# Performance work log

Measured on AMD Instinct MI355X. Metric: run time of the kernel, lower is better.

Reference implementation:

```python
import jax, jax.numpy as jnp
import numpy as np

K = 20          # knn neighbors (args.k)
BN_EPS = 1e-5   # torch BatchNorm default
LN_EPS = 1e-6


def _bn(x, g, b, axes):
    # training-mode batchnorm over `axes`, channel dim = 1
    m = x.mean(axes, keepdims=True)
    v = x.var(axes, keepdims=True)
    shp = [1] * x.ndim
    shp[1] = x.shape[1]
    return g.reshape(shp) * (x - m) * jax.lax.rsqrt(v + BN_EPS) + b.reshape(shp)


def _lrelu(x):
    return jnp.where(x >= 0, x, 0.2 * x)


def _graph_feature(x, k):
    # x: [B,C,N] -> [B,2C,N,k]  (knn gather + (neighbor-center, center) concat)
    B, C, N = x.shape
    inner = -2.0 * jnp.einsum('bcn,bcm->bnm', x, x)
    xx = jnp.sum(x * x, axis=1)                       # [B,N]
    pd = -xx[:, :, None] - inner - xx[:, None, :]     # negative sq. distance
    idx = jax.lax.top_k(pd, k)[1]                     # [B,N,k]
    xt = jnp.transpose(x, (0, 2, 1))                  # [B,N,C]
    feat = xt[jnp.arange(B)[:, None, None], idx]      # [B,N,k,C] gather
    ctr = xt[:, :, None, :]
    out = jnp.concatenate([feat - ctr, jnp.broadcast_to(ctr, feat.shape)], axis=-1)
    return jnp.transpose(out, (0, 3, 1, 2))


def _conv2d_block(x, w, g, b):
    # 1x1 conv2d (no bias) + BN2d + LeakyReLU(0.2)
    y = jnp.einsum('bcnk,oc->bonk', x, w)
    return _lrelu(_bn(y, g, b, (0, 2, 3)))


def _conv1d_block(x, w, g, b):
    y = jnp.einsum('bcl,oc->bol', x, w)
    return _lrelu(_bn(y, g, b, (0, 2)))


def _squash(t):
    sn = jnp.sum(t * t, axis=-1, keepdims=True)
    return sn * t / ((1.0 + sn) * jnp.sqrt(sn))


def _forward(data, l, dw1, dg1, db1, dw2, dg2, db2, dw3, dg3, db3,
             lin_w, ln_w, ln_b, caps_W,
             cw1, cg1, cb1, cw2, cg2, cb2, cw3, cw4, cg4, cb4, cw5, cg5, cb5):
    B, _, N = data.shape
    # ---- DGCNN encoder ----
    x = _conv2d_block(_graph_feature(data, K), dw1, dg1, db1)
    x1 = x.max(axis=-1)                               # [B,64,N]
    x = _conv2d_block(_graph_feature(x1, K), dw2, dg2, db2)
    x2 = x.max(axis=-1)                               # [B,64,N]
    x = _conv2d_block(_graph_feature(x2, K), dw3, dg3, db3)
    x3 = x.max(axis=-1)                               # [B,128,N]
    feat = jnp.transpose(jnp.concatenate([x1, x2, x3], axis=1), (0, 2, 1))  # [B,N,256]
    h = jnp.einsum('bnc,oc->bno', feat, lin_w)        # [B,N,40]
    mu = h.mean(axis=(1, 2), keepdims=True)
    var = h.var(axis=(1, 2), keepdims=True)
    encoder = jax.nn.relu(ln_w * (h - mu) * jax.lax.rsqrt(var + LN_EPS) + ln_b)  # [B,1024,40]
    # ---- Latent capsule layer (3-iter dynamic routing) ----
    u_hat = jnp.einsum('lpvd,bpd->blpv', caps_W, encoder)  # [B,40,1024,64]
    u_det = jax.lax.stop_gradient(u_hat)
    b_ij = jnp.zeros((B, caps_W.shape[0], caps_W.shape[1]), encoder.dtype)
    v = None
    for it in range(3):
        c = jax.nn.softmax(b_ij, axis=1)
        if it == 2:
            v = _squash(jnp.einsum('blp,blpv->blv', c, u_hat))
        else:
            v = _squash(jnp.einsum('blp,blpv->blv', c, u_det))
            b_ij = b_ij + jnp.einsum('blv,blpv->blp', v, u_det)
    latent = v                                        # [B,40,64]
    # ---- segmentation head ----
    emb = jnp.einsum('bpd,bdv->bpv', encoder, latent) # [B,1024,64]
    emb = emb.max(axis=-1, keepdims=True)             # [B,1024,1]
    lab = _conv1d_block(l.reshape(B, -1, 1), cw1, cg1, cb1)  # [B,64,1]
    emb = jnp.concatenate([emb, lab], axis=1)         # [B,1088,1]
    emb = jnp.tile(emb, (1, 1, N))                    # [B,1088,N]
    emb = jnp.concatenate([emb, jnp.transpose(encoder, (0, 2, 1))], axis=1)  # [B,1128,N]
    r = _conv1d_block(emb, cw2, cg2, cb2)
    r = _conv1d_block(r, cw3, cg2, cb2)               # conv3 shares bn2 params
    r = _conv1d_block(r, cw4, cg4, cb4)
    r = _conv1d_block(r, cw5, cg5, cb5)
    return r                                          # [B,50,N]


def setup_inputs() -> dict:
    key = jax.random.key(0)
    ks = jax.random.split(key, 16)
    B, N = 32, 1024
    f = jnp.float32
    rn = lambda k, s: 0.05 * jax.random.normal(k, s, dtype=f)
    return dict(
        data=jax.random.normal(ks[0], (B, 3, N), dtype=f),
        l=jax.random.uniform(ks[1], (B, 16), dtype=f),
        dw1=rn(ks[2], (64, 6)), dg1=jnp.ones(64, f), db1=jnp.zeros(64, f),
        dw2=rn(ks[3], (64, 128)), dg2=jnp.ones(64, f), db2=jnp.zeros(64, f),
        dw3=rn(ks[4], (128, 128)), dg3=jnp.ones(128, f), db3=jnp.zeros(128, f),
        lin_w=rn(ks[5], (40, 256)),
        ln_w=jnp.ones((N, 40), f), ln_b=jnp.zeros((N, 40), f),
        caps_W=0.01 * jax.random.normal(ks[6], (40, 1024, 64, 40), dtype=f),
        cw1=rn(ks[7], (64, 16)), cg1=jnp.ones(64, f), cb1=jnp.zeros(64, f),
        cw2=rn(ks[8], (256, 1128)), cg2=jnp.ones(256, f), cb2=jnp.zeros(256, f),
        cw3=rn(ks[9], (256, 256)),
        cw4=rn(ks[10], (128, 256)), cg4=jnp.ones(128, f), cb4=jnp.zeros(128, f),
        cw5=rn(ks[11], (50, 128)), cg5=jnp.ones(50, f), cb5=jnp.zeros(50, f),
    )


def reference(data, l, dw1, dg1, db1, dw2, dg2, db2, dw3, dg3, db3,
              lin_w, ln_w, ln_b, caps_W,
              cw1, cg1, cb1, cw2, cg2, cb2, cw3, cw4, cg4, cb4, cw5, cg5, cb5):
    return _forward(data, l, dw1, dg1, db1, dw2, dg2, db2, dw3, dg3, db3,
                    lin_w, ln_w, ln_b, caps_W,
                    cw1, cg1, cb1, cw2, cg2, cb2, cw3, cw4, cg4, cb4, cw5, cg5, cb5)
```

## Files before the change

kernel.cpp:

```cpp
#include <hip/hip_runtime.h>
#include <math.h>

constexpr int NB = 32, NN = 1024, KNN = 20;
constexpr int RTOT = NB * NN;

constexpr size_t SZ_BIG = (size_t)NB * NN * 40 * 64;
constexpr size_t O_BIG  = 0;
constexpr size_t O_XT0  = O_BIG + SZ_BIG;
constexpr size_t O_XT1  = O_XT0 + (size_t)RTOT * 4;
constexpr size_t O_XT2  = O_XT1 + (size_t)RTOT * 64;
constexpr size_t O_XT3  = O_XT2 + (size_t)RTOT * 64;
constexpr size_t O_XX   = O_XT3 + (size_t)RTOT * 128;
constexpr size_t O_IDX  = O_XX + RTOT;
constexpr size_t O_WC1  = O_IDX + (size_t)RTOT * KNN;
constexpr size_t O_WC2  = O_WC1 + 512;
constexpr size_t O_WC3  = O_WC2 + 8192;
constexpr size_t O_LWT  = O_WC3 + 16384;
constexpr size_t O_C2T  = O_LWT + 16384;
constexpr size_t O_C3T  = O_C2T + 10240;
constexpr size_t O_C4T  = O_C3T + 65536;
constexpr size_t O_C5T  = O_C4T + 32768;
constexpr size_t O_H    = O_C5T + 8192;
constexpr size_t O_LNST = O_H + (size_t)RTOT * 64;
constexpr size_t O_BSUM = O_LNST + 64;
constexpr size_t O_BSQ  = O_BSUM + 256;
constexpr size_t O_SCL  = O_BSQ + 256;
constexpr size_t O_SHF  = O_SCL + 256;
constexpr size_t O_SACC = O_SHF + 256;
constexpr size_t O_VB   = O_SACC + 81920;
constexpr size_t O_BIJ  = O_VB + 81920;
constexpr size_t O_EMB  = O_BIJ + (size_t)NB * 40 * NN;
constexpr size_t O_LAB  = O_EMB + RTOT;
constexpr size_t O_BASE = O_LAB + 2048;
constexpr size_t O_PS   = O_BIJ;
constexpr size_t O_PQ   = O_BIJ + 262144;
constexpr size_t O_PB   = O_XT1;

__device__ __forceinline__ float lrelu(float z) { return fmaxf(z, 0.2f * z); }

__device__ __forceinline__ float key2f(unsigned u)
{
    unsigned b = (u & 0x80000000u) ? (u ^ 0x80000000u) : ~u;
    return __uint_as_float(b);
}

__global__ void k_wt(const float* __restrict__ src, float* __restrict__ dst,
                     int K, int On, int SS, int coff, int DS, int ooff, int Oreal)
{
    int i = blockIdx.x * 256 + threadIdx.x;
    if (i >= K * On) return;
    int c = i / On, o = i - c * On;
    dst[(size_t)c * DS + ooff + o] = (o < Oreal) ? src[(size_t)o * SS + coff + c] : 0.f;
}

__global__ void k_data_t(const float* __restrict__ d, float* __restrict__ xt)
{
    int i = blockIdx.x * 256 + threadIdx.x;
    if (i >= RTOT) return;
    int b = i >> 10, n = i & 1023;
#pragma unroll
    for (int c = 0; c < 3; ++c) xt[(size_t)i * 4 + c] = d[((size_t)b * 3 + c) * NN + n];
    xt[(size_t)i * 4 + 3] = 0.f;
}

template<int C, int CS>
__global__ void k_rownorm(const float* __restrict__ X, float* __restrict__ xx)
{
    int i = blockIdx.x * 256 + threadIdx.x;
    if (i >= RTOT) return;
    const float* p = X + (size_t)i * CS;
    float s = 0.f;
#pragma unroll
    for (int c = 0; c < C; ++c) s = fmaf(p[c], p[c], s);
    xx[i] = s;
}

template<int CS>
__global__ __launch_bounds__(256) void k_dist(const float* __restrict__ X,
    const float* __restrict__ xx, float* __restrict__ D)
{
    __shared__ float As[16][68];
    __shared__ float Bs[16][68];
    int b = blockIdx.z;
    int r0 = blockIdx.x * 64, m0 = blockIdx.y * 64;
    const float* Xb = X + (size_t)b * NN * CS;
    int t = threadIdx.x;
    int tx = t & 15, ty = t >> 4;
    float acc[4][4] = {};
    for (int k0 = 0; k0 < CS; k0 += 16) {
        __syncthreads();
        {
            int row = t >> 2, kb = (t & 3) * 4;
#pragma unroll
            for (int u = 0; u < 4; ++u) {
                int k = k0 + kb + u;
                As[kb + u][row] = (k < CS) ? Xb[(size_t)(r0 + row) * CS + k] : 0.f;
                Bs[kb + u][row] = (k < CS) ? Xb[(size_t)(m0 + row) * CS + k] : 0.f;
            }
        }
        __syncthreads();
#pragma unroll
        for (int k = 0; k < 16; ++k) {
            float4 a = *(const float4*)&As[k][ty * 4];
            float4 bb = *(const float4*)&Bs[k][tx * 4];
            float av[4] = {a.x, a.y, a.z, a.w};
            float bv[4] = {bb.x, bb.y, bb.z, bb.w};
#pragma unroll
            for (int i = 0; i < 4; ++i)
#pragma unroll
                for (int j = 0; j < 4; ++j)
                    acc[i][j] = fmaf(av[i], bv[j], acc[i][j]);
        }
    }
    const float* xxb = xx + b * NN + m0 + tx * 4;
    float x0 = xxb[0], x1 = xxb[1], x2 = xxb[2], x3 = xxb[3];
#pragma unroll
    for (int i = 0; i < 4; ++i) {
        float4 o4 = make_float4(2.f * acc[i][0] - x0, 2.f * acc[i][1] - x1,
                                2.f * acc[i][2] - x2, 2.f * acc[i][3] - x3);
        *(float4*)&D[((size_t)b * NN + r0 + ty * 4 + i) * NN + m0 + tx * 4] = o4;
    }
}

__global__ __launch_bounds__(256) void k_sel(const float* __restrict__ D,
                                             int* __restrict__ idxb)
{
    int gw = blockIdx.x * 4 + (threadIdx.x >> 6);
    int lane = threadIdx.x & 63;
    const float* drow = D + (size_t)gw * NN;
    float vr[16];
#pragma unroll
    for (int j = 0; j < 16; ++j) vr[j] = drow[j * 64 + lane];

    unsigned lo = 0x007FFFFFu;
    unsigned hi = 0xFF800000u;
#pragma unroll 1
    while (hi - lo > 1u) {
        unsigned mid = lo + ((hi - lo) >> 1);
        float tm = key2f(mid);
        int c = 0;
#pragma unroll
        for (int j = 0; j < 16; ++j) c += __popcll(__ballot(vr[j] > tm));
        if (c < KNN) hi = mid; else lo = mid;
    }
    float t = key2f(hi);

    int* outp = idxb + (size_t)gw * KNN;
    unsigned long long mylow = (1ull << lane) - 1ull;
    int base = 0;
#pragma unroll
    for (int j = 0; j < 16; ++j) {
        unsigned long long bmask = __ballot(vr[j] > t);
        if (vr[j] > t) outp[base + __popcll(bmask & mylow)] = j * 64 + lane;
        base += __popcll(bmask);
    }
#pragma unroll 1
    for (int j = 0; j < 16 && base < KNN; ++j) {
        unsigned long long bmask = __ballot(vr[j] == t);
        int pre = __popcll(bmask & mylow);
        if (vr[j] == t && base + pre < KNN) outp[base + pre] = j * 64 + lane;
        base += __popcll(bmask);
    }
}

template<bool ACT, bool BIAS>
__global__ __launch_bounds__(256) void k_gemm(const float* __restrict__ X,
    const float* __restrict__ W, float* __restrict__ Y, int K, int OC, int XS,
    const float* __restrict__ scale, const float* __restrict__ shift,
    const float* __restrict__ bias)
{
    __shared__ float Xs[16][68];
    __shared__ float Ws[16][64];
    int r0 = blockIdx.x * 64, o0 = blockIdx.y * 64;
    int t = threadIdx.x;
    int tx = t & 15, ty = t >> 4;
    float acc[4][4] = {};
    for (int k0 = 0; k0 < K; k0 += 16) {
        __syncthreads();
        {
            int row = t >> 2, kb = (t & 3) * 4;
#pragma unroll
            for (int u = 0; u < 4; ++u) {
                int k = k0 + kb + u;
                float v = 0.f;
                if (k < K) {
                    v = X[(size_t)(r0 + row) * XS + k];
                    if (ACT) { float z = fmaf(v, scale[k], shift[k]); v = fmaxf(z, 0.2f * z); }
                }
                Xs[kb + u][row] = v;
// ... 31 lines not shown
        *(float4*)&Y[(size_t)r * OC + o0 + tx * 4] = o4;
    }
}

template<int O>
__global__ __launch_bounds__(256) void k_gather(const float* __restrict__ Z,
    const int* __restrict__ idxb, float* __restrict__ xo,
    float* __restrict__ part_s, float* __restrict__ part_q)
{
    constexpr int OL = O / 64;
    __shared__ float rs[4][O], rq[4][O];
    int b = blockIdx.y, nt = blockIdx.x;
    int t = threadIdx.x, lane = t & 63, w = t >> 6;
    float ps[OL] = {}, pq[OL] = {};
    for (int i = 0; i < 4; ++i) {
        int n = nt * 16 + w * 4 + i;
        size_t r = (size_t)b * NN + n;
        float zd[OL], ym[OL];
#pragma unroll
        for (int j = 0; j < OL; ++j) {
            int o = lane + j * 64;
            zd[j] = Z[r * (2 * O) + O + o] - Z[r * (2 * O) + o];
            ym[j] = -3.4e38f;
        }
        int midx[KNN];
        {
            const int4* ip = (const int4*)&idxb[r * KNN];
#pragma unroll
            for (int q = 0; q < 5; ++q) {
                int4 t4 = ip[q];
                midx[4 * q + 0] = t4.x; midx[4 * q + 1] = t4.y;
                midx[4 * q + 2] = t4.z; midx[4 * q + 3] = t4.w;
            }
        }
#pragma unroll
        for (int k = 0; k < KNN; ++k) {
            size_t rm = (size_t)b * NN + midx[k];
#pragma unroll
            for (int j = 0; j < OL; ++j) {
                float y = Z[rm * (2 * O) + lane + j * 64] + zd[j];
                ym[j] = fmaxf(ym[j], y);
                ps[j] += y; pq[j] = fmaf(y, y, pq[j]);
            }
        }
#pragma unroll
        for (int j = 0; j < OL; ++j) xo[r * O + lane + j * 64] = ym[j];
    }
#pragma unroll
    for (int j = 0; j < OL; ++j) { rs[w][lane + j * 64] = ps[j]; rq[w][lane + j * 64] = pq[j]; }
    __syncthreads();
    if (w == 0) {
        int blk = blockIdx.y * 64 + blockIdx.x;
#pragma unroll
        for (int j = 0; j < OL; ++j) {
            int o = lane + j * 64;
            part_s[(size_t)o * 2048 + blk] = rs[0][o] + rs[1][o] + rs[2][o] + rs[3][o];
            part_q[(size_t)o * 2048 + blk] = rq[0][o] + rq[1][o] + rq[2][o] + rq[3][o];
        }
    }
}

__global__ void k_bnfin2(const float* __restrict__ part_s, const float* __restrict__ part_q,
                         const float* __restrict__ g, const float* __restrict__ bb,
                         float* __restrict__ scale, float* __restrict__ shift,
                         int OC, float invM, float eps)
{
    int o = blockIdx.x * blockDim.x + threadIdx.x;
    if (o >= OC) return;
    const float* ps = part_s + (size_t)o * 2048;
    const float* pq = part_q + (size_t)o * 2048;
    float s0 = 0.f, s1 = 0.f, s2 = 0.f, s3 = 0.f;
    float q0 = 0.f, q1 = 0.f, q2 = 0.f, q3 = 0.f;
    for (int i = 0; i < 2048; i += 4) {
        s0 += ps[i]; s1 += ps[i + 1]; s2 += ps[i + 2]; s3 += ps[i + 3];
        q0 += pq[i]; q1 += pq[i + 1]; q2 += pq[i + 2]; q3 += pq[i + 3];
    }
    float s = (s0 + s1) + (s2 + s3);
    float q = (q0 + q1) + (q2 + q3);
    float mu = s * invM;
    float var = q * invM - mu * mu;
    float sc = g[o] * rsqrtf(var + eps);
    scale[o] = sc; shift[o] = bb[o] - mu * sc;
}

__global__ void k_bnfin(const float* __restrict__ sums, const float* __restrict__ sumsq,
                        const float* __restrict__ g, const float* __restrict__ bb,
                        float* __restrict__ scale, float* __restrict__ shift,
                        int OC, float invM, float eps)
{
    int o = blockIdx.x * blockDim.x + threadIdx.x;
    if (o >= OC) return;
    float mu = sums[o] * invM;
    float var = sumsq[o] * invM - mu * mu;
    float sc = g[o] * rsqrtf(var + eps);
    scale[o] = sc; shift[o] = bb[o] - mu * sc;
}

__global__ void k_bnapply(float* __restrict__ x, const float* __restrict__ scale,
                          const float* __restrict__ shift, int total, int O)
{
    int i = blockIdx.x * 256 + threadIdx.x;
    if (i >= total) return;
    int o = i & (O - 1);
    x[i] = lrelu(fmaf(x[i], scale[o], shift[o]));
}

__global__ void k_concat(const float* __restrict__ x1, const float* __restrict__ x2,
                         const float* __restrict__ x3, float* __restrict__ f)
{
    int i = blockIdx.x * 256 + threadIdx.x;
    if (i >= RTOT * 256) return;
    int r = i >> 8, c = i & 255;
    float v;
    if (c < 64) v = x1[(size_t)r * 64 + c];
    else if (c < 128) v = x2[(size_t)r * 64 + c - 64];
    else v = x3[(size_t)r * 128 + c - 128];
    f[(size_t)i] = v;
}

__global__ __launch_bounds__(256) void k_lnstats(const float* __restrict__ h, float* __restrict__ st)
{
    __shared__ float rsm[256], rqm[256];
    int b = blockIdx.x, t = threadIdx.x;
    float s = 0.f, q = 0.f;
    for (int i = t; i < 40960; i += 256) {
        int n = i / 40, o = i - n * 40;
        float v = h[((size_t)b * NN + n) * 64 + o];
        s += v; q = fmaf(v, v, q);
    }
    rsm[t] = s; rqm[t] = q; __syncthreads();
    for (int off = 128; off; off >>= 1) {
        if (t < off) { rsm[t] += rsm[t + off]; rqm[t] += rqm[t + off]; }
        __syncthreads();
    }
    if (t == 0) {
        float mu = rsm[0] / 40960.f;
        float var = rqm[0] / 40960.f - mu * mu;
        st[2 * b] = mu; st[2 * b + 1] = rsqrtf(var + 1e-6f);
    }
}

__global__ void k_lnapply(float* __restrict__ h, const float* __restrict__ lnw,
                          const float* __restrict__ lnb, const float* __restrict__ st)
{
    int i = blockIdx.x * 256 + threadIdx.x;
    if (i >= NB * NN * 40) return;
    int b = i / 40960, rem = i - b * 40960, n = rem / 40, o = rem - n * 40;
    float mu = st[2 * b], rstd = st[2 * b + 1];
    size_t a = ((size_t)b * NN + n) * 64 + o;
    float v = fmaf((h[a] - mu) * rstd, lnw[n * 40 + o], lnb[n * 40 + o]);
    h[a] = fmaxf(v, 0.f);
}

__global__ __launch_bounds__(64) void k_uhat(const float* __restrict__ enc,
    const float* __restrict__ caps, float* __restrict__ U)
{
    __shared__ float clt[40 * 68];
    int p = blockIdx.x, l = blockIdx.y, t = threadIdx.x;
    const float4* cp4 = (const float4*)(caps + ((size_t)l * NN + p) * 2560);
#pragma unroll
    for (int k = 0; k < 10; ++k) {
        int i4 = t + k * 64;
        float4 cv = cp4[i4];
        int e0 = i4 * 4;
        int v = e0 / 40;
        int d0 = e0 - v * 40;
        clt[(d0 + 0) * 68 + v] = cv.x;
        clt[(d0 + 1) * 68 + v] = cv.y;
        clt[(d0 + 2) * 68 + v] = cv.z;
        clt[(d0 + 3) * 68 + v] = cv.w;
    }
    __syncthreads();
    int vg = t & 7, bg = t >> 3;
    int v0 = vg * 8, b0 = bg * 4;
    float acc[4][8] = {};
#pragma unroll
    for (int d4 = 0; d4 < 10; ++d4) {
        float4 e4[4];
#pragma unroll
        for (int i = 0; i < 4; ++i)
            e4[i] = *(const float4*)&enc[((size_t)(b0 + i) * NN + p) * 64 + d4 * 4];
#pragma unroll
        for (int dd = 0; dd < 4; ++dd) {
            int d = d4 * 4 + dd;
            float4 c0 = *(const float4*)&clt[d * 68 + v0];
            float4 c1 = *(const float4*)&clt[d * 68 + v0 + 4];
            float cv[8] = {c0.x, c0.y, c0.z, c0.w, c1.x, c1.y, c1.z, c1.w};
#pragma unroll
            for (int i = 0; i < 4; ++i) {
                float e = ((const float*)&e4[i])[dd];
#pragma unroll
                for (int j = 0; j < 8; ++j)
                    acc[i][j] = fmaf(e, cv[j], acc[i][j]);
            }
        }
    }
#pragma unroll
    for (int i = 0; i < 4; ++i) {
        float* up = &U[((size_t)(b0 + i) * NN + p) * 2560 + l * 64 + v0];
        float4 o0 = make_float4(acc[i][0], acc[i][1], acc[i][2], acc[i][3]);
        float4 o1 = make_float4(acc[i][4], acc[i][5], acc[i][6], acc[i][7]);
        *(float4*)up = o0;
        *(float4*)(up + 4) = o1;
    }
}

template<int MODE>
__global__ __launch_bounds__(256, 4) void k_route(const float* __restrict__ U,
    const float* __restrict__ vprev, const float* __restrict__ bin,
    float* __restrict__ bout, float* __restrict__ pbuf)
{
    __shared__ float vl[2560];
    __shared__ float red[4][1280];
    int b = blockIdx.x, pc = blockIdx.y;
    int t = threadIdx.x, lane = t & 63, w = t >> 6;
    if (MODE != 0) {
        for (int i = t; i < 2560; i += 256) vl[i] = vprev[(size_t)b * 2560 + i];
        __syncthreads();
    }
    float4 acc[10];
#pragma unroll
    for (int it = 0; it < 10; ++it) acc[it] = make_float4(0.f, 0.f, 0.f, 0.f);
    int lgrp = lane >> 4;
#pragma unroll 1
    for (int pi = 0; pi < 8; ++pi) {
        int p = pc * 32 + w * 8 + pi;
        const float4* up4 = (const float4*)(U + ((size_t)b * NN + p) * 2560);
        float4 u[10];
#pragma unroll
        for (int it = 0; it < 10; ++it) u[it] = up4[it * 64 + lane];
        if (MODE == 0) {
#pragma unroll
            for (int it = 0; it < 10; ++it) {
                acc[it].x += u[it].x; acc[it].y += u[it].y;
                acc[it].z += u[it].z; acc[it].w += u[it].w;
            }
        } else {
            float pd[10];
#pragma unroll
            for (int it = 0; it < 10; ++it) {
                float4 vv = *(const float4*)&vl[it * 256 + lane * 4];
                float s = u[it].x * vv.x;
                s = fmaf(u[it].y, vv.y, s);
                s = fmaf(u[it].z, vv.z, s);
                s = fmaf(u[it].w, vv.w, s);
                s += __shfl_xor(s, 1, 64);
                s += __shfl_xor(s, 2, 64);
                s += __shfl_xor(s, 4, 64);
                s += __shfl_xor(s, 8, 64);
                pd[it] = s;
            }
            if (MODE == 1) {
                if ((lane & 15) == 0) {
#pragma unroll
                    for (int it = 0; it < 10; ++it)
                        bout[((size_t)b * 40 + it * 4 + lgrp) * NN + p] = pd[it];
                }
            } else {
#pragma unroll
                for (int it = 0; it < 10; ++it)
                    pd[it] += bin[((size_t)b * 40 + it * 4 + lgrp) * NN + p];
            }
            float mx = -3.4e38f;
#pragma unroll
            for (int it = 0; it < 10; ++it) {
                float m = pd[it];
                m = fmaxf(m, __shfl_xor(m, 16, 64));
                m = fmaxf(m, __shfl_xor(m, 32, 64));
                mx = fmaxf(mx, m);
            }
            float eo[10]; float se = 0.f;
#pragma unroll
            for (int it = 0; it < 10; ++it) {
                float e = expf(pd[it] - mx);
                eo[it] = e;
                float sg = e;
                sg += __shfl_xor(sg, 16, 64);
                sg += __shfl_xor(sg, 32, 64);
                se += sg;
            }
            float inv = 1.f / se;
#pragma unroll
            for (int it = 0; it < 10; ++it) {
                float wgt = eo[it] * inv;
                acc[it].x = fmaf(wgt, u[it].x, acc[it].x);
                acc[it].y = fmaf(wgt, u[it].y, acc[it].y);
                acc[it].z = fmaf(wgt, u[it].z, acc[it].z);
                acc[it].w = fmaf(wgt, u[it].w, acc[it].w);
            }
        }
    }
    float* pb = pbuf + ((size_t)pc * NB + b) * 2560;
#pragma unroll 1
    for (int h = 0; h < 2; ++h) {
        __syncthreads();
#pragma unroll
        for (int it = 0; it < 5; ++it)
            *(float4*)&red[w][it * 256 + lane * 4] = acc[h * 5 + it];
        __syncthreads();
        if (w == 0) {
#pragma unroll
            for (int it = 0; it < 5; ++it) {
                int idx = it * 256 + lane * 4;
                float4 a0 = *(const float4*)&red[0][idx];
                float4 a1 = *(const float4*)&red[1][idx];
                float4 a2 = *(const float4*)&red[2][idx];
                float4 a3 = *(const float4*)&red[3][idx];
                float4 o = make_float4((a0.x + a1.x) + (a2.x + a3.x),
                                       (a0.y + a1.y) + (a2.y + a3.y),
                                       (a0.z + a1.z) + (a2.z + a3.z),
                                       (a0.w + a1.w) + (a2.w + a3.w));
                *(float4*)&pb[h * 1280 + idx] = o;
            }
        }
    }
}

__global__ void k_sred(const float* __restrict__ pbuf, float* __restrict__ sac)
{
    int i4 = blockIdx.x * 256 + threadIdx.x;
    if (i4 >= NB * 640) return;
    const float4* pb4 = (const float4*)pbuf;
    float4 s = make_float4(0.f, 0.f, 0.f, 0.f);
#pragma unroll 4
    for (int pc = 0; pc < 32; ++pc) {
        float4 v = pb4[(size_t)pc * (NB * 640) + i4];
        s.x += v.x; s.y += v.y; s.z += v.z; s.w += v.w;
    }
    ((float4*)sac)[i4] = s;
}

__global__ void k_squash(const float* __restrict__ s_in, float* __restrict__ vout, float premul)
{
    int i = blockIdx.x * 256 + threadIdx.x;
    if (i >= NB * 40) return;
    const float* sp = s_in + (size_t)i * 64;
    float* vp = vout + (size_t)i * 64;
    float sn = 0.f;
    for (int v = 0; v < 64; ++v) { float tv = sp[v] * premul; sn = fmaf(tv, tv, sn); }
    float f = sn / ((1.f + sn) * sqrtf(sn));
    for (int v = 0; v < 64; ++v) vp[v] = sp[v] * premul * f;
}

__global__ __launch_bounds__(256) void k_emb(const float* __restrict__ enc,
    const float* __restrict__ lat, float* __restrict__ embm)
{
    __shared__ float latl[2560];
    int b = blockIdx.x, pt = blockIdx.y;
    int t = threadIdx.x, lane = t & 63, w = t >> 6;
    for (int i = t; i < 2560; i += 256) latl[i] = lat[(size_t)b * 2560 + i];
    __syncthreads();
    for (int i = 0; i < 32; ++i) {
        int p = pt * 128 + w * 32 + i;
        const float* ep = enc + ((size_t)b * NN + p) * 64;
        float acc = 0.f;
#pragma unroll
        for (int d = 0; d < 40; ++d) acc = fmaf(ep[d], latl[d * 64 + lane], acc);
        float mx = acc;
#pragma unroll
        for (int s = 32; s; s >>= 1) mx = fmaxf(mx, __shfl_xor(mx, s, 64));
        if (lane == 0) embm[(size_t)b * NN + p] = mx;
    }
}

__global__ __launch_bounds__(64) void k_lab(const float* __restrict__ lin,
    const float* __restrict__ w, const float* __restrict__ g, const float* __restrict__ bb,
    float* __restrict__ lab)
{
    int o = threadIdx.x;
    float ys[32]; float s = 0.f, q = 0.f;
#pragma unroll
    for (int b = 0; b < 32; ++b) {
        float y = 0.f;
#pragma unroll
        for (int c = 0; c < 16; ++c) y = fmaf(lin[b * 16 + c], w[o * 16 + c], y);
        ys[b] = y; s += y; q = fmaf(y, y, q);
    }
    float mu = s / 32.f, var = q / 32.f - mu * mu;
    float sc = g[o] * rsqrtf(var + 1e-5f);
    float sh = bb[o] - mu * sc;
#pragma unroll
    for (int b = 0; b < 32; ++b) lab[b * 64 + o] = lrelu(fmaf(ys[b], sc, sh));
}

__global__ __launch_bounds__(256) void k_base2(const float* __restrict__ em,
    const float* __restrict__ lab, const float* __restrict__ cw2, float* __restrict__ base)
{
    __shared__ float eml[1024];
    __shared__ float lbl[64];
    int b = blockIdx.x, t = threadIdx.x;
    for (int i = t; i < 1024; i += 256) eml[i] = em[(size_t)b * NN + i];
    if (t < 64) lbl[t] = lab[b * 64 + t];
    __syncthreads();
    const float* wr = cw2 + (size_t)t * 1128;
    float acc = 0.f;
    for (int c = 0; c < 1024; ++c) acc = fmaf(wr[c], eml[c], acc);
#pragma unroll
    for (int c = 0; c < 64; ++c) acc = fmaf(wr[1024 + c], lbl[c], acc);
    base[b * 256 + t] = acc;
}

__global__ __launch_bounds__(256) void k_colstats(const float* __restrict__ Y,
    float* __restrict__ sums, float* __restrict__ sumsq, int OC)
{
    __shared__ float rs[4][64], rq[4][64];
    int chunk = blockIdx.x, o0 = blockIdx.y * 64;
    int t = threadIdx.x, lane = t & 63, w = t >> 6;
    int o = o0 + lane;
    float s = 0.f, q = 0.f;
    for (int j = 0; j < 64; ++j) {
        int r = chunk * 256 + w * 64 + j;
        float v = Y[(size_t)r * OC + o];
        s += v; q = fmaf(v, v, q);
    }
    rs[w][lane] = s; rq[w][lane] = q;
    __syncthreads();
    if (w == 0) {
        atomicAdd(&sums[o], rs[0][lane] + rs[1][lane] + rs[2][lane] + rs[3][lane]);
        atomicAdd(&sumsq[o], rq[0][lane] + rq[1][lane] + rq[2][lane] + rq[3][lane]);
    }
}

__global__ void k_out(const float* __restrict__ Y, const float* __restrict__ scale,
                      const float* __restrict__ shift, float* __restrict__ out)
{
    int i = blockIdx.x * 256 + threadIdx.x;
    if (i >= NB * 50 * NN) return;
    int n = i & 1023, rest = i >> 10;
    int o = rest % 50, b = rest / 50;
    float y = Y[((size_t)b * NN + n) * 64 + o];
    out[i] = lrelu(fmaf(y, scale[o], shift[o]));
}

extern "C" void kernel_launch(void* const* d_in, const int* in_sizes, int n_in,
                              void* d_out, int out_size, void* d_ws, size_t ws_size,
                              hipStream_t stream)
{
    const float* data = (const float*)d_in[0];
    const float* lin  = (const float*)d_in[1];
    const float* dw1  = (const float*)d_in[2];
    const float* dg1  = (const float*)d_in[3];
    const float* db1  = (const float*)d_in[4];
    const float* dw2  = (const float*)d_in[5];
    const float* dg2  = (const float*)d_in[6];
    const float* db2  = (const float*)d_in[7];
    const float* dw3  = (const float*)d_in[8];
    const float* dg3  = (const float*)d_in[9];
    const float* db3  = (const float*)d_in[10];
    const float* lw   = (const float*)d_in[11];
    const float* lnw  = (const float*)d_in[12];
    const float* lnb  = (const float*)d_in[13];
    const float* caps = (const float*)d_in[14];
    const float* cw1  = (const float*)d_in[15];
    const float* cg1  = (const float*)d_in[16];
    const float* cb1  = (const float*)d_in[17];
    const float* cw2  = (const float*)d_in[18];
    const float* cg2  = (const float*)d_in[19];
    const float* cb2  = (const float*)d_in[20];
    const float* cw3  = (const float*)d_in[21];
    const float* cw4  = (const float*)d_in[22];
    const float* cg4  = (const float*)d_in[23];
    const float* cb4  = (const float*)d_in[24];
    const float* cw5  = (const float*)d_in[25];
    const float* cg5  = (const float*)d_in[26];
    const float* cb5  = (const float*)d_in[27];
    float* out = (float*)d_out;
    float* ws = (float*)d_ws;

    float* big  = ws + O_BIG;
    float* xt0  = ws + O_XT0;
    float* xt1  = ws + O_XT1;
    float* xt2  = ws + O_XT2;
    float* xt3  = ws + O_XT3;
    float* xxp  = ws + O_XX;
    int*   idxb = (int*)(ws + O_IDX);
    float* wc1  = ws + O_WC1;
    float* wc2  = ws + O_WC2;
    float* wc3  = ws + O_WC3;
    float* lwt  = ws + O_LWT;
    float* c2t  = ws + O_C2T;
    float* c3t  = ws + O_C3T;
    float* c4t  = ws + O_C4T;
    float* c5t  = ws + O_C5T;
    float* hbuf = ws + O_H;
    float* lnst = ws + O_LNST;
    float* bsum = ws + O_BSUM;
    float* bsq  = ws + O_BSQ;
    float* scl  = ws + O_SCL;
    float* shf  = ws + O_SHF;
    float* sac  = ws + O_SACC;
    float* vb   = ws + O_VB;
    float* bij  = ws + O_BIJ;
    float* embm = ws + O_EMB;
    float* labp = ws + O_LAB;
    float* basep= ws + O_BASE;
    float* psP  = ws + O_PS;
    float* pqP  = ws + O_PQ;
    float* pbuf = ws + O_PB;
    float* Dbuf = big;
    float* Z    = big;
    float* U    = big;
    float* yb1  = big;
    float* yb2  = big + 8388608;

    k_wt<<<1,   256, 0, stream>>>(dw1, wc1, 3, 64, 6, 0, 128, 0, 64);
    k_wt<<<1,   256, 0, stream>>>(dw1, wc1, 3, 64, 6, 3, 128, 64, 64);
    k_wt<<<16,  256, 0, stream>>>(dw2, wc2, 64, 64, 128, 0, 128, 0, 64);
    k_wt<<<16,  256, 0, stream>>>(dw2, wc2, 64, 64, 128, 64, 128, 64, 64);
    k_wt<<<32,  256, 0, stream>>>(dw3, wc3, 64, 128, 128, 0, 256, 0, 128);
    k_wt<<<32,  256, 0, stream>>>(dw3, wc3, 64, 128, 128, 64, 256, 128, 128);
    k_wt<<<64,  256, 0, stream>>>(lw,  lwt, 256, 64, 256, 0, 64, 0, 40);
    k_wt<<<40,  256, 0, stream>>>(cw2, c2t, 40, 256, 1128, 1088, 256, 0, 256);
    k_wt<<<256, 256, 0, stream>>>(cw3, c3t, 256, 256, 256, 0, 256, 0, 256);
    k_wt<<<128, 256, 0, stream>>>(cw4, c4t, 256, 128, 256, 0, 128, 0, 128);
    k_wt<<<32,  256, 0, stream>>>(cw5, c5t, 128, 64, 128, 0, 64, 0, 50);
    k_data_t<<<128, 256, 0, stream>>>(data, xt0);

    k_rownorm<3, 4><<<128, 256, 0, stream>>>(xt0, xxp);
    k_dist<4><<<dim3(16, 16, 32), 256, 0, stream>>>(xt0, xxp, Dbuf);
    k_sel<<<8192, 256, 0, stream>>>(Dbuf, idxb);
    k_gemm<false, false><<<dim3(512, 2), 256, 0, stream>>>(xt0, wc1, Z, 3, 128, 4, nullptr, nullptr, nullptr);
    k_gather<64><<<dim3(64, 32), 256, 0, stream>>>(Z, idxb, xt1, psP, pqP);
    k_bnfin2<<<1, 64, 0, stream>>>(psP, pqP, dg1, db1, scl, shf, 64, 1.f / 655360.f, 1e-5f);
    k_bnapply<<<8192, 256, 0, stream>>>(xt1, scl, shf, RTOT * 64, 64);

    k_rownorm<64, 64><<<128, 256, 0, stream>>>(xt1, xxp);
    k_dist<64><<<dim3(16, 16, 32), 256, 0, stream>>>(xt1, xxp, Dbuf);
    k_sel<<<8192, 256, 0, stream>>>(Dbuf, idxb);
    k_gemm<false, false><<<dim3(512, 2), 256, 0, stream>>>(xt1, wc2, Z, 64, 128, 64, nullptr, nullptr, nullptr);
    k_gather<64><<<dim3(64, 32), 256, 0, stream>>>(Z, idxb, xt2, psP, pqP);
    k_bnfin2<<<1, 64, 0, stream>>>(psP, pqP, dg2, db2, scl, shf, 64, 1.f / 655360.f, 1e-5f);
    k_bnapply<<<8192, 256, 0, stream>>>(xt2, scl, shf, RTOT * 64, 64);

    k_rownorm<64, 64><<<128, 256, 0, stream>>>(xt2, xxp);
    k_dist<64><<<dim3(16, 16, 32), 256, 0, stream>>>(xt2, xxp, Dbuf);
    k_sel<<<8192, 256, 0, stream>>>(Dbuf, idxb);
    k_gemm<false, false><<<dim3(512, 4), 256, 0, stream>>>(xt2, wc3, Z, 64, 256, 64, nullptr, nullptr, nullptr);
    k_gather<128><<<dim3(64, 32), 256, 0, stream>>>(Z, idxb, xt3, psP, pqP);
    k_bnfin2<<<1, 128, 0, stream>>>(psP, pqP, dg3, db3, scl, shf, 128, 1.f / 655360.f, 1e-5f);
    k_bnapply<<<16384, 256, 0, stream>>>(xt3, scl, shf, RTOT * 128, 128);

    k_concat<<<32768, 256, 0, stream>>>(xt1, xt2, xt3, big);
    k_gemm<false, false><<<dim3(512, 1), 256, 0, stream>>>(big, lwt, hbuf, 256, 64, 256, nullptr, nullptr, nullptr);
    k_lnstats<<<32, 256, 0, stream>>>(hbuf, lnst);
    k_lnapply<<<5120, 256, 0, stream>>>(hbuf, lnw, lnb, lnst);

    k_uhat<<<dim3(1024, 40), 64, 0, stream>>>(hbuf, caps, U);
    k_route<0><<<dim3(32, 32), 256, 0, stream>>>(U, nullptr, nullptr, nullptr, pbuf);
    k_sred<<<80, 256, 0, stream>>>(pbuf, sac);
    k_squash<<<5, 256, 0, stream>>>(sac, vb, 1.f / 40.f);
    k_route<1><<<dim3(32, 32), 256, 0, stream>>>(U, vb, nullptr, bij, pbuf);
    k_sred<<<80, 256, 0, stream>>>(pbuf, sac);
    k_squash<<<5, 256, 0, stream>>>(sac, vb, 1.f);
    k_route<2><<<dim3(32, 32), 256, 0, stream>>>(U, vb, bij, nullptr, pbuf);
    k_sred<<<80, 256, 0, stream>>>(pbuf, sac);
    k_squash<<<5, 256, 0, stream>>>(sac, vb, 1.f);

    k_emb<<<dim3(32, 8), 256, 0, stream>>>(hbuf, vb, embm);
    k_lab<<<1, 64, 0, stream>>>(lin, cw1, cg1, cb1, labp);
    k_base2<<<32, 256, 0, stream>>>(embm, labp, cw2, basep);

    k_gemm<false, true><<<dim3(512, 4), 256, 0, stream>>>(hbuf, c2t, yb1, 40, 256, 64, nullptr, nullptr, basep);
    hipMemsetAsync(bsum, 0, 512 * 4, stream);
    k_colstats<<<dim3(128, 4), 256, 0, stream>>>(yb1, bsum, bsq, 256);
    k_bnfin<<<1, 256, 0, stream>>>(bsum, bsq, cg2, cb2, scl, shf, 256, 1.f / 32768.f, 1e-5f);

    k_gemm<true, false><<<dim3(512, 4), 256, 0, stream>>>(yb1, c3t, yb2, 256, 256, 256, scl, shf, nullptr);
    hipMemsetAsync(bsum, 0, 512 * 4, stream);
    k_colstats<<<dim3(128, 4), 256, 0, stream>>>(yb2, bsum, bsq, 256);
    k_bnfin<<<1, 256, 0, stream>>>(bsum, bsq, cg2, cb2, scl, shf, 256, 1.f / 32768.f, 1e-5f);

    k_gemm<true, false><<<dim3(512, 2), 256, 0, stream>>>(yb2, c4t, yb1, 256, 128, 256, scl, shf, nullptr);
    hipMemsetAsync(bsum, 0, 512 * 4, stream);
    k_colstats<<<dim3(128, 2), 256, 0, stream>>>(yb1, bsum, bsq, 128);
    k_bnfin<<<1, 256, 0, stream>>>(bsum, bsq, cg4, cb4, scl, shf, 128, 1.f / 32768.f, 1e-5f);

    k_gemm<true, false><<<dim3(512, 1), 256, 0, stream>>>(yb1, c5t, yb2, 128, 64, 128, scl, shf, nullptr);
    hipMemsetAsync(bsum, 0, 512 * 4, stream);
    k_colstats<<<dim3(128, 1), 256, 0, stream>>>(yb2, bsum, bsq, 64);
    k_bnfin<<<1, 256, 0, stream>>>(bsum, bsq, cg5, cb5, scl, shf, 50, 1.f / 32768.f, 1e-5f);

    k_out<<<6400, 256, 0, stream>>>(yb2, scl, shf, out);
}
```

Before: 1.822 ms.

## Fuse first routing sum into u_hat kernel and drop route mode zero

The u_hat kernel now handles 16 points per block, two waves each looping over 8 points, and accumulates per-block partial sums of U over points. Those partials are written to a per-chunk buffer, which replaces the separate k_route<0> pass that re-read the whole U tensor only to sum it. The reduction kernel is templated on chunk count to handle 64 chunks for the fused path and 32 for the later passes. In exchange the u_hat grid is much smaller, giving less parallelism and serialising the caps loads within each wave, and it adds a partial-sum buffer that aliases the xt1 region.

```diff
diff --git a/kernel.cpp b/kernel.cpp
--- a/kernel.cpp
+++ b/kernel.cpp
@@ -35,6 +35,7 @@
 constexpr size_t O_PS   = O_BIJ;
 constexpr size_t O_PQ   = O_BIJ + 262144;
 constexpr size_t O_PB   = O_XT1;
+constexpr size_t O_PBU  = O_XT1;
 
 __device__ __forceinline__ float lrelu(float z) { return fmaxf(z, 0.2f * z); }
 
@@ -372,56 +373,83 @@
     h[a] = fmaxf(v, 0.f);
 }
 
-__global__ __launch_bounds__(64) void k_uhat(const float* __restrict__ enc,
-    const float* __restrict__ caps, float* __restrict__ U)
-{
-    __shared__ float clt[40 * 68];
-    int p = blockIdx.x, l = blockIdx.y, t = threadIdx.x;
-    const float4* cp4 = (const float4*)(caps + ((size_t)l * NN + p) * 2560);
-#pragma unroll
-    for (int k = 0; k < 10; ++k) {
-        int i4 = t + k * 64;
-        float4 cv = cp4[i4];
-        int e0 = i4 * 4;
-        int v = e0 / 40;
-        int d0 = e0 - v * 40;
-        clt[(d0 + 0) * 68 + v] = cv.x;
-        clt[(d0 + 1) * 68 + v] = cv.y;
-        clt[(d0 + 2) * 68 + v] = cv.z;
-        clt[(d0 + 3) * 68 + v] = cv.w;
+__global__ __launch_bounds__(128) void k_uhat(const float* __restrict__ enc,
+    const float* __restrict__ caps, float* __restrict__ U, float* __restrict__ pbu)
+{
+    __shared__ float clt[2][40 * 68];
+    __shared__ float red[2048];
+    int pc = blockIdx.x, l = blockIdx.y;
+    int t = threadIdx.x, lane = t & 63, wv = t >> 6;
+    int vg = lane & 7, bg = lane >> 3;
+    int v0 = vg * 8, b0 = bg * 4;
+    float* cw = clt[wv];
+    float spart[4][8] = {};
+#pragma unroll 1
+    for (int pi = 0; pi < 8; ++pi) {
+        int p = pc * 16 + wv * 8 + pi;
+        const float4* cp4 = (const float4*)(caps + ((size_t)l * NN + p) * 2560);
+#pragma unroll
+        for (int k = 0; k < 10; ++k) {
+            int i4 = lane + k * 64;
+            float4 cv = cp4[i4];
+            int e0 = i4 * 4;
+            int v = e0 / 40;
+            int d0 = e0 - v * 40;
+            cw[(d0 + 0) * 68 + v] = cv.x;
+            cw[(d0 + 1) * 68 + v] = cv.y;
+            cw[(d0 + 2) * 68 + v] = cv.z;
+            cw[(d0 + 3) * 68 + v] = cv.w;
+        }
+        float acc[4][8] = {};
+#pragma unroll
+        for (int d4 = 0; d4 < 10; ++d4) {
+            float4 e4[4];
+#pragma unroll
+            for (int i = 0; i < 4; ++i)
+                e4[i] = *(const float4*)&enc[((size_t)(b0 + i) * NN + p) * 64 + d4 * 4];
+#pragma unroll
+            for (int dd = 0; dd < 4; ++dd) {
+                int d = d4 * 4 + dd;
+                float4 c0 = *(const float4*)&cw[d * 68 + v0];
+                float4 c1 = *(const float4*)&cw[d * 68 + v0 + 4];
+                float cv[8] = {c0.x, c0.y, c0.z, c0.w, c1.x, c1.y, c1.z, c1.w};
+#pragma unroll
+                for (int i = 0; i < 4; ++i) {
+                    float e = ((const float*)&e4[i])[dd];
+#pragma unroll
+                    for (int j = 0; j < 8; ++j)
+                        acc[i][j] = fmaf(e, cv[j], acc[i][j]);
+                }
+            }
+        }
+#pragma unroll
+        for (int i = 0; i < 4; ++i) {
+            float* up = &U[((size_t)(b0 + i) * NN + p) * 2560 + l * 64 + v0];
+            float4 o0 = make_float4(acc[i][0], acc[i][1], acc[i][2], acc[i][3]);
+            float4 o1 = make_float4(acc[i][4], acc[i][5], acc[i][6], acc[i][7]);
+            *(float4*)up = o0;
+            *(float4*)(up + 4) = o1;
+#pragma unroll
+            for (int j = 0; j < 8; ++j) spart[i][j] += acc[i][j];
+        }
+    }
+    if (wv == 1) {
+#pragma unroll
+        for (int i = 0; i < 4; ++i)
+#pragma unroll
+            for (int j = 0; j < 8; ++j)
+                red[(b0 + i) * 64 + v0 + j] = spart[i][j];
     }
     __syncthreads();
-    int vg = t & 7, bg = t >> 3;
-    int v0 = vg * 8, b0 = bg * 4;
-    float acc[4][8] = {};
-#pragma unroll
-    for (int d4 = 0; d4 < 10; ++d4) {
-        float4 e4[4];
+    if (wv == 0) {
+        float* pb = pbu + (size_t)pc * 81920;
 #pragma unroll
         for (int i = 0; i < 4; ++i)
-            e4[i] = *(const float4*)&enc[((size_t)(b0 + i) * NN + p) * 64 + d4 * 4];
-#pragma unroll
-        for (int dd = 0; dd < 4; ++dd) {
-            int d = d4 * 4 + dd;
-            float4 c0 = *(const float4*)&clt[d * 68 + v0];
-            float4 c1 = *(const float4*)&clt[d * 68 + v0 + 4];
-            float cv[8] = {c0.x, c0.y, c0.z, c0.w, c1.x, c1.y, c1.z, c1.w};
-#pragma unroll
-            for (int i = 0; i < 4; ++i) {
-                float e = ((const float*)&e4[i])[dd];
-#pragma unroll
-                for (int j = 0; j < 8; ++j)
-                    acc[i][j] = fmaf(e, cv[j], acc[i][j]);
+#pragma unroll
+            for (int j = 0; j < 8; ++j) {
+                int bv = (b0 + i) * 64 + v0 + j;
+                pb[(size_t)(b0 + i) * 2560 + l * 64 + v0 + j] = spart[i][j] + red[bv];
             }
-        }
-    }
-#pragma unroll
-    for (int i = 0; i < 4; ++i) {
-        float* up = &U[((size_t)(b0 + i) * NN + p) * 2560 + l * 64 + v0];
-        float4 o0 = make_float4(acc[i][0], acc[i][1], acc[i][2], acc[i][3]);
-        float4 o1 = make_float4(acc[i][4], acc[i][5], acc[i][6], acc[i][7]);
-        *(float4*)up = o0;
-        *(float4*)(up + 4) = o1;
     }
 }
 
@@ -434,10 +462,8 @@
     __shared__ float red[4][1280];
     int b = blockIdx.x, pc = blockIdx.y;
     int t = threadIdx.x, lane = t & 63, w = t >> 6;
-    if (MODE != 0) {
-        for (int i = t; i < 2560; i += 256) vl[i] = vprev[(size_t)b * 2560 + i];
-        __syncthreads();
-    }
+    for (int i = t; i < 2560; i += 256) vl[i] = vprev[(size_t)b * 2560 + i];
+    __syncthreads();
     float4 acc[10];
 #pragma unroll
     for (int it = 0; it < 10; ++it) acc[it] = make_float4(0.f, 0.f, 0.f, 0.f);
@@ -449,65 +475,57 @@
         float4 u[10];
 #pragma unroll
         for (int it = 0; it < 10; ++it) u[it] = up4[it * 64 + lane];
-        if (MODE == 0) {
-#pragma unroll
-            for (int it = 0; it < 10; ++it) {
-                acc[it].x += u[it].x; acc[it].y += u[it].y;
-                acc[it].z += u[it].z; acc[it].w += u[it].w;
+        float pd[10];
+#pragma unroll
+        for (int it = 0; it < 10; ++it) {
+            float4 vv = *(const float4*)&vl[it * 256 + lane * 4];
+            float s = u[it].x * vv.x;
+            s = fmaf(u[it].y, vv.y, s);
+            s = fmaf(u[it].z, vv.z, s);
+            s = fmaf(u[it].w, vv.w, s);
+            s += __shfl_xor(s, 1, 64);
+            s += __shfl_xor(s, 2, 64);
+            s += __shfl_xor(s, 4, 64);
+            s += __shfl_xor(s, 8, 64);
+            pd[it] = s;
+        }
+        if (MODE == 1) {
+            if ((lane & 15) == 0) {
+#pragma unroll
+                for (int it = 0; it < 10; ++it)
+                    bout[((size_t)b * 40 + it * 4 + lgrp) * NN + p] = pd[it];
             }
         } else {
-            float pd[10];
-#pragma unroll
-            for (int it = 0; it < 10; ++it) {
-                float4 vv = *(const float4*)&vl[it * 256 + lane * 4];
-                float s = u[it].x * vv.x;
-                s = fmaf(u[it].y, vv.y, s);
-                s = fmaf(u[it].z, vv.z, s);
-                s = fmaf(u[it].w, vv.w, s);
-                s += __shfl_xor(s, 1, 64);
-                s += __shfl_xor(s, 2, 64);
-                s += __shfl_xor(s, 4, 64);
-                s += __shfl_xor(s, 8, 64);
-                pd[it] = s;
-            }
-            if (MODE == 1) {
-                if ((lane & 15) == 0) {
-#pragma unroll
-                    for (int it = 0; it < 10; ++it)
-                        bout[((size_t)b * 40 + it * 4 + lgrp) * NN + p] = pd[it];
-                }
-            } else {
-#pragma unroll
-                for (int it = 0; it < 10; ++it)
-                    pd[it] += bin[((size_t)b * 40 + it * 4 + lgrp) * NN + p];
-            }
-            float mx = -3.4e38f;
-#pragma unroll
-            for (int it = 0; it < 10; ++it) {
-                float m = pd[it];
-                m = fmaxf(m, __shfl_xor(m, 16, 64));
-                m = fmaxf(m, __shfl_xor(m, 32, 64));
-                mx = fmaxf(mx, m);
-            }
-            float eo[10]; float se = 0.f;
-#pragma unroll
-            for (int it = 0; it < 10; ++it) {
-                float e = expf(pd[it] - mx);
-                eo[it] = e;
-                float sg = e;
-                sg += __shfl_xor(sg, 16, 64);
-                sg += __shfl_xor(sg, 32, 64);
-                se += sg;
-            }
-            float inv = 1.f / se;
-#pragma unroll
-            for (int it = 0; it < 10; ++it) {
-                float wgt = eo[it] * inv;
-                acc[it].x = fmaf(wgt, u[it].x, acc[it].x);
-                acc[it].y = fmaf(wgt, u[it].y, acc[it].y);
-                acc[it].z = fmaf(wgt, u[it].z, acc[it].z);
-                acc[it].w = fmaf(wgt, u[it].w, acc[it].w);
-            }
+#pragma unroll
+            for (int it = 0; it < 10; ++it)
+                pd[it] += bin[((size_t)b * 40 + it * 4 + lgrp) * NN + p];
+        }
+        float mx = -3.4e38f;
+#pragma unroll
+        for (int it = 0; it < 10; ++it) {
+            float m = pd[it];
+            m = fmaxf(m, __shfl_xor(m, 16, 64));
+            m = fmaxf(m, __shfl_xor(m, 32, 64));
+            mx = fmaxf(mx, m);
+        }
+        float eo[10]; float se = 0.f;
+#pragma unroll
+        for (int it = 0; it < 10; ++it) {
+            float e = expf(pd[it] - mx);
+            eo[it] = e;
+            float sg = e;
+            sg += __shfl_xor(sg, 16, 64);
+            sg += __shfl_xor(sg, 32, 64);
+            se += sg;
+        }
+        float inv = 1.f / se;
+#pragma unroll
+        for (int it = 0; it < 10; ++it) {
+            float wgt = eo[it] * inv;
+            acc[it].x = fmaf(wgt, u[it].x, acc[it].x);
+            acc[it].y = fmaf(wgt, u[it].y, acc[it].y);
+            acc[it].z = fmaf(wgt, u[it].z, acc[it].z);
+            acc[it].w = fmaf(wgt, u[it].w, acc[it].w);
         }
     }
     float* pb = pbuf + ((size_t)pc * NB + b) * 2560;
@@ -536,14 +554,15 @@
     }
 }
 
-__global__ void k_sred(const float* __restrict__ pbuf, float* __restrict__ sac)
+template<int NCH>
+__global__ void k_sredN(const float* __restrict__ pbuf, float* __restrict__ sac)
 {
     int i4 = blockIdx.x * 256 + threadIdx.x;
     if (i4 >= NB * 640) return;
     const float4* pb4 = (const float4*)pbuf;
     float4 s = make_float4(0.f, 0.f, 0.f, 0.f);
 #pragma unroll 4
-    for (int pc = 0; pc < 32; ++pc) {
+    for (int pc = 0; pc < NCH; ++pc) {
         float4 v = pb4[(size_t)pc * (NB * 640) + i4];
         s.x += v.x; s.y += v.y; s.z += v.z; s.w += v.w;
     }
@@ -717,6 +736,7 @@
     float* psP  = ws + O_PS;
     float* pqP  = ws + O_PQ;
     float* pbuf = ws + O_PB;
+    float* pbu  = ws + O_PBU;
     float* Dbuf = big;
     float* Z    = big;
     float* U    = big;
@@ -765,15 +785,14 @@
     k_lnstats<<<32, 256, 0, stream>>>(hbuf, lnst);
     k_lnapply<<<5120, 256, 0, stream>>>(hbuf, lnw, lnb, lnst);
 
-    k_uhat<<<dim3(1024, 40), 64, 0, stream>>>(hbuf, caps, U);
-    k_route<0><<<dim3(32, 32), 256, 0, stream>>>(U, nullptr, nullptr, nullptr, pbuf);
-    k_sred<<<80, 256, 0, stream>>>(pbuf, sac);
+    k_uhat<<<dim3(64, 40), 128, 0, stream>>>(hbuf, caps, U, pbu);
+    k_sredN<64><<<80, 256, 0, stream>>>(pbu, sac);
     k_squash<<<5, 256, 0, stream>>>(sac, vb, 1.f / 40.f);
     k_route<1><<<dim3(32, 32), 256, 0, stream>>>(U, vb, nullptr, bij, pbuf);
-    k_sred<<<80, 256, 0, stream>>>(pbuf, sac);
+    k_sredN<32><<<80, 256, 0, stream>>>(pbuf, sac);
     k_squash<<<5, 256, 0, stream>>>(sac, vb, 1.f);
     k_route<2><<<dim3(32, 32), 256, 0, stream>>>(U, vb, bij, nullptr, pbuf);
-    k_sred<<<80, 256, 0, stream>>>(pbuf, sac);
+    k_sredN<32><<<80, 256, 0, stream>>>(pbuf, sac);
     k_squash<<<5, 256, 0, stream>>>(sac, vb, 1.f);
 
     k_emb<<<dim3(32, 8), 256, 0, stream>>>(hbuf, vb, embm);
```

After: 1.765 ms. 3.1% less time.

## Fuse first routing-pass sum into u_hat kernel, dropping route mode 0

Applied to the files above, without the earlier changes.

The u_hat kernel now handles 16 points per block and accumulates per-chunk partial sums of U. Those sums are written to a partial buffer that a templated reduction consumes. This removes the separate first routing pass, which re-read the whole U tensor just to sum it. In exchange the u_hat grid shrinks sharply, which lowers parallelism and latency hiding. The per-iteration shared-memory staging also runs without a barrier, relying on the block being a single wavefront.

```diff
diff --git a/kernel.cpp b/kernel.cpp
--- a/kernel.cpp
+++ b/kernel.cpp
@@ -35,6 +35,7 @@
 constexpr size_t O_PS   = O_BIJ;
 constexpr size_t O_PQ   = O_BIJ + 262144;
 constexpr size_t O_PB   = O_XT1;
+constexpr size_t O_PBU  = O_XT1;
 
 __device__ __forceinline__ float lrelu(float z) { return fmaxf(z, 0.2f * z); }
 
@@ -373,55 +374,71 @@
 }
 
 __global__ __launch_bounds__(64) void k_uhat(const float* __restrict__ enc,
-    const float* __restrict__ caps, float* __restrict__ U)
+    const float* __restrict__ caps, float* __restrict__ U, float* __restrict__ pbu)
 {
     __shared__ float clt[40 * 68];
-    int p = blockIdx.x, l = blockIdx.y, t = threadIdx.x;
-    const float4* cp4 = (const float4*)(caps + ((size_t)l * NN + p) * 2560);
-#pragma unroll
-    for (int k = 0; k < 10; ++k) {
-        int i4 = t + k * 64;
-        float4 cv = cp4[i4];
-        int e0 = i4 * 4;
-        int v = e0 / 40;
-        int d0 = e0 - v * 40;
-        clt[(d0 + 0) * 68 + v] = cv.x;
-        clt[(d0 + 1) * 68 + v] = cv.y;
-        clt[(d0 + 2) * 68 + v] = cv.z;
-        clt[(d0 + 3) * 68 + v] = cv.w;
-    }
-    __syncthreads();
-    int vg = t & 7, bg = t >> 3;
+    int pc = blockIdx.x, l = blockIdx.y;
+    int lane = threadIdx.x;
+    int vg = lane & 7, bg = lane >> 3;
     int v0 = vg * 8, b0 = bg * 4;
-    float acc[4][8] = {};
-#pragma unroll
-    for (int d4 = 0; d4 < 10; ++d4) {
-        float4 e4[4];
-#pragma unroll
-        for (int i = 0; i < 4; ++i)
-            e4[i] = *(const float4*)&enc[((size_t)(b0 + i) * NN + p) * 64 + d4 * 4];
-#pragma unroll
-        for (int dd = 0; dd < 4; ++dd) {
-            int d = d4 * 4 + dd;
-            float4 c0 = *(const float4*)&clt[d * 68 + v0];
-            float4 c1 = *(const float4*)&clt[d * 68 + v0 + 4];
-            float cv[8] = {c0.x, c0.y, c0.z, c0.w, c1.x, c1.y, c1.z, c1.w};
-#pragma unroll
-            for (int i = 0; i < 4; ++i) {
-                float e = ((const float*)&e4[i])[dd];
-#pragma unroll
-                for (int j = 0; j < 8; ++j)
-                    acc[i][j] = fmaf(e, cv[j], acc[i][j]);
+    float spart[4][8] = {};
+#pragma unroll 1
+    for (int pi = 0; pi < 16; ++pi) {
+        int p = pc * 16 + pi;
+        const float4* cp4 = (const float4*)(caps + ((size_t)l * NN + p) * 2560);
+#pragma unroll
+        for (int k = 0; k < 10; ++k) {
+            int i4 = lane + k * 64;
+            float4 cv = cp4[i4];
+            int e0 = i4 * 4;
+            int v = e0 / 40;
+            int d0 = e0 - v * 40;
+            clt[(d0 + 0) * 68 + v] = cv.x;
+            clt[(d0 + 1) * 68 + v] = cv.y;
+            clt[(d0 + 2) * 68 + v] = cv.z;
+            clt[(d0 + 3) * 68 + v] = cv.w;
+        }
+        float acc[4][8] = {};
+#pragma unroll
+        for (int d4 = 0; d4 < 10; ++d4) {
+            float4 e4[4];
+#pragma unroll
+            for (int i = 0; i < 4; ++i)
+                e4[i] = *(const float4*)&enc[((size_t)(b0 + i) * NN + p) * 64 + d4 * 4];
+#pragma unroll
+            for (int dd = 0; dd < 4; ++dd) {
+                int d = d4 * 4 + dd;
+                float4 c0 = *(const float4*)&clt[d * 68 + v0];
+                float4 c1 = *(const float4*)&clt[d * 68 + v0 + 4];
+                float cv[8] = {c0.x, c0.y, c0.z, c0.w, c1.x, c1.y, c1.z, c1.w};
+#pragma unroll
+                for (int i = 0; i < 4; ++i) {
+                    float e = ((const float*)&e4[i])[dd];
+#pragma unroll
+                    for (int j = 0; j < 8; ++j)
+                        acc[i][j] = fmaf(e, cv[j], acc[i][j]);
+                }
             }
         }
-    }
+#pragma unroll
+        for (int i = 0; i < 4; ++i) {
+            float* up = &U[((size_t)(b0 + i) * NN + p) * 2560 + l * 64 + v0];
+            float4 o0 = make_float4(acc[i][0], acc[i][1], acc[i][2], acc[i][3]);
+            float4 o1 = make_float4(acc[i][4], acc[i][5], acc[i][6], acc[i][7]);
+            *(float4*)up = o0;
+            *(float4*)(up + 4) = o1;
+#pragma unroll
+            for (int j = 0; j < 8; ++j) spart[i][j] += acc[i][j];
+        }
+    }
+    float* pb = pbu + (size_t)pc * 81920;
 #pragma unroll
     for (int i = 0; i < 4; ++i) {
-        float* up = &U[((size_t)(b0 + i) * NN + p) * 2560 + l * 64 + v0];
-        float4 o0 = make_float4(acc[i][0], acc[i][1], acc[i][2], acc[i][3]);
-        float4 o1 = make_float4(acc[i][4], acc[i][5], acc[i][6], acc[i][7]);
-        *(float4*)up = o0;
-        *(float4*)(up + 4) = o1;
+        float4 s0 = make_float4(spart[i][0], spart[i][1], spart[i][2], spart[i][3]);
+        float4 s1 = make_float4(spart[i][4], spart[i][5], spart[i][6], spart[i][7]);
+        float* dst = &pb[(size_t)(b0 + i) * 2560 + l * 64 + v0];
+        *(float4*)dst = s0;
+        *(float4*)(dst + 4) = s1;
     }
 }
 
@@ -434,10 +451,8 @@
     __shared__ float red[4][1280];
     int b = blockIdx.x, pc = blockIdx.y;
     int t = threadIdx.x, lane = t & 63, w = t >> 6;
-    if (MODE != 0) {
-        for (int i = t; i < 2560; i += 256) vl[i] = vprev[(size_t)b * 2560 + i];
-        __syncthreads();
-    }
+    for (int i = t; i < 2560; i += 256) vl[i] = vprev[(size_t)b * 2560 + i];
+    __syncthreads();
     float4 acc[10];
 #pragma unroll
     for (int it = 0; it < 10; ++it) acc[it] = make_float4(0.f, 0.f, 0.f, 0.f);
@@ -449,65 +464,57 @@
         float4 u[10];
 #pragma unroll
         for (int it = 0; it < 10; ++it) u[it] = up4[it * 64 + lane];
-        if (MODE == 0) {
-#pragma unroll
-            for (int it = 0; it < 10; ++it) {
-                acc[it].x += u[it].x; acc[it].y += u[it].y;
-                acc[it].z += u[it].z; acc[it].w += u[it].w;
+        float pd[10];
+#pragma unroll
+        for (int it = 0; it < 10; ++it) {
+            float4 vv = *(const float4*)&vl[it * 256 + lane * 4];
+            float s = u[it].x * vv.x;
+            s = fmaf(u[it].y, vv.y, s);
+            s = fmaf(u[it].z, vv.z, s);
+            s = fmaf(u[it].w, vv.w, s);
+            s += __shfl_xor(s, 1, 64);
+            s += __shfl_xor(s, 2, 64);
+            s += __shfl_xor(s, 4, 64);
+            s += __shfl_xor(s, 8, 64);
+            pd[it] = s;
+        }
+        if (MODE == 1) {
+            if ((lane & 15) == 0) {
+#pragma unroll
+                for (int it = 0; it < 10; ++it)
+                    bout[((size_t)b * 40 + it * 4 + lgrp) * NN + p] = pd[it];
             }
         } else {
-            float pd[10];
-#pragma unroll
-            for (int it = 0; it < 10; ++it) {
-                float4 vv = *(const float4*)&vl[it * 256 + lane * 4];
-                float s = u[it].x * vv.x;
-                s = fmaf(u[it].y, vv.y, s);
-                s = fmaf(u[it].z, vv.z, s);
-                s = fmaf(u[it].w, vv.w, s);
-                s += __shfl_xor(s, 1, 64);
-                s += __shfl_xor(s, 2, 64);
-                s += __shfl_xor(s, 4, 64);
-                s += __shfl_xor(s, 8, 64);
-                pd[it] = s;
-            }
-            if (MODE == 1) {
-                if ((lane & 15) == 0) {
-#pragma unroll
-                    for (int it = 0; it < 10; ++it)
-                        bout[((size_t)b * 40 + it * 4 + lgrp) * NN + p] = pd[it];
-                }
-            } else {
-#pragma unroll
-                for (int it = 0; it < 10; ++it)
-                    pd[it] += bin[((size_t)b * 40 + it * 4 + lgrp) * NN + p];
-            }
-            float mx = -3.4e38f;
-#pragma unroll
-            for (int it = 0; it < 10; ++it) {
-                float m = pd[it];
-                m = fmaxf(m, __shfl_xor(m, 16, 64));
-                m = fmaxf(m, __shfl_xor(m, 32, 64));
-                mx = fmaxf(mx, m);
-            }
-            float eo[10]; float se = 0.f;
-#pragma unroll
-            for (int it = 0; it < 10; ++it) {
-                float e = expf(pd[it] - mx);
-                eo[it] = e;
-                float sg = e;
-                sg += __shfl_xor(sg, 16, 64);
-                sg += __shfl_xor(sg, 32, 64);
-                se += sg;
-            }
-            float inv = 1.f / se;
-#pragma unroll
-            for (int it = 0; it < 10; ++it) {
-                float wgt = eo[it] * inv;
-                acc[it].x = fmaf(wgt, u[it].x, acc[it].x);
-                acc[it].y = fmaf(wgt, u[it].y, acc[it].y);
-                acc[it].z = fmaf(wgt, u[it].z, acc[it].z);
-                acc[it].w = fmaf(wgt, u[it].w, acc[it].w);
-            }
+#pragma unroll
+            for (int it = 0; it < 10; ++it)
+                pd[it] += bin[((size_t)b * 40 + it * 4 + lgrp) * NN + p];
+        }
+        float mx = -3.4e38f;
+#pragma unroll
+        for (int it = 0; it < 10; ++it) {
+            float m = pd[it];
+            m = fmaxf(m, __shfl_xor(m, 16, 64));
+            m = fmaxf(m, __shfl_xor(m, 32, 64));
+            mx = fmaxf(mx, m);
+        }
+        float eo[10]; float se = 0.f;
+#pragma unroll
+        for (int it = 0; it < 10; ++it) {
+            float e = expf(pd[it] - mx);
+            eo[it] = e;
+            float sg = e;
+            sg += __shfl_xor(sg, 16, 64);
+            sg += __shfl_xor(sg, 32, 64);
+            se += sg;
+        }
+        float inv = 1.f / se;
+#pragma unroll
+        for (int it = 0; it < 10; ++it) {
+            float wgt = eo[it] * inv;
+            acc[it].x = fmaf(wgt, u[it].x, acc[it].x);
+            acc[it].y = fmaf(wgt, u[it].y, acc[it].y);
+            acc[it].z = fmaf(wgt, u[it].z, acc[it].z);
+            acc[it].w = fmaf(wgt, u[it].w, acc[it].w);
         }
     }
     float* pb = pbuf + ((size_t)pc * NB + b) * 2560;
@@ -536,14 +543,15 @@
     }
 }
 
-__global__ void k_sred(const float* __restrict__ pbuf, float* __restrict__ sac)
+template<int NCH>
+__global__ void k_sredN(const float* __restrict__ pbuf, float* __restrict__ sac)
 {
     int i4 = blockIdx.x * 256 + threadIdx.x;
     if (i4 >= NB * 640) return;
     const float4* pb4 = (const float4*)pbuf;
     float4 s = make_float4(0.f, 0.f, 0.f, 0.f);
 #pragma unroll 4
-    for (int pc = 0; pc < 32; ++pc) {
+    for (int pc = 0; pc < NCH; ++pc) {
         float4 v = pb4[(size_t)pc * (NB * 640) + i4];
         s.x += v.x; s.y += v.y; s.z += v.z; s.w += v.w;
     }
@@ -717,6 +725,7 @@
     float* psP  = ws + O_PS;
     float* pqP  = ws + O_PQ;
     float* pbuf = ws + O_PB;
+    float* pbu  = ws + O_PBU;
     float* Dbuf = big;
     float* Z    = big;
     float* U    = big;
@@ -765,15 +774,14 @@
     k_lnstats<<<32, 256, 0, stream>>>(hbuf, lnst);
     k_lnapply<<<5120, 256, 0, stream>>>(hbuf, lnw, lnb, lnst);
 
-    k_uhat<<<dim3(1024, 40), 64, 0, stream>>>(hbuf, caps, U);
-    k_route<0><<<dim3(32, 32), 256, 0, stream>>>(U, nullptr, nullptr, nullptr, pbuf);
-    k_sred<<<80, 256, 0, stream>>>(pbuf, sac);
+    k_uhat<<<dim3(64, 40), 64, 0, stream>>>(hbuf, caps, U, pbu);
+    k_sredN<64><<<80, 256, 0, stream>>>(pbu, sac);
     k_squash<<<5, 256, 0, stream>>>(sac, vb, 1.f / 40.f);
     k_route<1><<<dim3(32, 32), 256, 0, stream>>>(U, vb, nullptr, bij, pbuf);
-    k_sred<<<80, 256, 0, stream>>>(pbuf, sac);
+    k_sredN<32><<<80, 256, 0, stream>>>(pbuf, sac);
     k_squash<<<5, 256, 0, stream>>>(sac, vb, 1.f);
     k_route<2><<<dim3(32, 32), 256, 0, stream>>>(U, vb, bij, nullptr, pbuf);
-    k_sred<<<80, 256, 0, stream>>>(pbuf, sac);
+    k_sredN<32><<<80, 256, 0, stream>>>(pbuf, sac);
     k_squash<<<5, 256, 0, stream>>>(sac, vb, 1.f);
 
     k_emb<<<dim3(32, 8), 256, 0, stream>>>(hbuf, vb, embm);
```

After: 1.755 ms. 1.04x faster.
